# Optimization experiments

Measured on AMD Instinct MI355X. Metric: run time of the kernel, lower is better.

## Reference

```python
import jax, jax.numpy as jnp
import numpy as np

H = 16  # num_heads (d_model=1024, d_head=64)


def setup_inputs() -> dict:
    key = jax.random.key(0)
    ks = jax.random.split(key, 10)
    B, L, S, G, D = 8, 1024, 1024, 64, 1024
    s = 0.02  # keep score magnitudes sane for softmax
    return {
        "queries": jax.random.normal(ks[0], (B, L, D), jnp.float32),
        "keys": jax.random.normal(ks[1], (B, S, D), jnp.float32),
        "values": jax.random.normal(ks[2], (B, S, D), jnp.float32),
        "routers": jax.random.normal(ks[3], (B, G, D), jnp.float32),
        "Wq": jax.random.normal(ks[4], (D, D), jnp.float32) * s,
        "Wk": jax.random.normal(ks[5], (D, D), jnp.float32) * s,
        "Wv": jax.random.normal(ks[6], (D, D), jnp.float32) * s,
        "Wlq": jax.random.normal(ks[7], (D, D), jnp.float32) * s,
        "Wlk": jax.random.normal(ks[8], (D, D), jnp.float32) * s,
        "Wo": jax.random.normal(ks[9], (D, D), jnp.float32) * s,
        "bo": jnp.zeros((D,), jnp.float32),
    }


def reference(queries, keys, values, routers, Wq, Wk, Wv, Wlq, Wlk, Wo, bo):
    B, L, _ = queries.shape
    S = keys.shape[1]
    d_head = queries.shape[-1] // H
    scale = d_head ** (-0.5)

    def split_heads(x, W, n):
        # (B,n,d_model) @ (d_model,H*d_head) -> (B,H,n,d_head)
        return (x @ W).reshape(B, n, H, d_head).transpose(0, 2, 1, 3)

    q = split_heads(queries, Wq, L)
    k = split_heads(keys, Wk, S)
    v = split_heads(values, Wv, S)
    rq = split_heads(routers, Wlq, routers.shape[1])
    rk = split_heads(routers, Wlk, routers.shape[1])

    # learned per-head bilinear electrode-position matrix: (B,H,d,d)
    W_ep = jnp.einsum('bhgd,bhge->bhde', rq, rk)
    # bilinear QK scores: q . W_ep . k^T
    scores = jnp.einsum('bhld,bhde,bhke->bhlk', q, W_ep, k) * scale
    attn = jax.nn.softmax(scores, axis=-1)  # (B,H,L,S)
    out = jnp.einsum('bhlk,bhkd->bhld', attn, v)  # (B,H,L,d_head)
    # faithful to original: transpose(-2,-1) then view(B,L,-1)
    out = jnp.swapaxes(out, -2, -1).reshape(B, L, H * d_head)
    return out @ Wo + bo
```

## Files before the change

### kernel.cpp

```cpp
#include <hip/hip_runtime.h>

typedef __bf16 bf16;
typedef short s8v __attribute__((ext_vector_type(8)));
typedef float f4v __attribute__((ext_vector_type(4)));
typedef bf16 bf4v __attribute__((ext_vector_type(4)));
typedef bf16 bf8v __attribute__((ext_vector_type(8)));

#define NH 16
#define BB 8
#define QWSCALE 0.18033688011112043f

__device__ __forceinline__ void glds16(void* lds, const void* g) {
    __builtin_amdgcn_global_load_lds(
        (const __attribute__((address_space(1))) unsigned int*)g,
        (__attribute__((address_space(3))) unsigned int*)lds, 16, 0, 0);
}

__global__ __launch_bounds__(256) void rgemm_k(
    const float* __restrict__ A, const float* __restrict__ W1, const float* __restrict__ W2,
    float* __restrict__ C1, float* __restrict__ C2)
{
    __shared__ float As[16][68];
    __shared__ float Bs[16][68];
    const int tid = threadIdx.x;
    const int bm = blockIdx.x;
    int bn = blockIdx.y;
    const float* W = (bn < 16) ? W1 : W2;
    float* C = (bn < 16) ? C1 : C2;
    if (bn >= 16) bn -= 16;
    const int n0 = bn * 64;

    const int ar = tid >> 2, ac = (tid & 3) * 4;
    const int br = tid >> 4, bc = (tid & 15) * 4;
    const int tr = (tid >> 4) * 4, tc = (tid & 15) * 4;

    float acc[4][4];
#pragma unroll
    for (int i = 0; i < 4; i++)
#pragma unroll
        for (int j = 0; j < 4; j++) acc[i][j] = 0.f;

    for (int kt = 0; kt < 1024; kt += 16) {
        float4 av = *(const float4*)&A[(size_t)(bm * 64 + ar) * 1024 + kt + ac];
        float4 bv = *(const float4*)&W[(size_t)(kt + br) * 1024 + n0 + bc];
        __syncthreads();
        As[ac + 0][ar] = av.x; As[ac + 1][ar] = av.y;
        As[ac + 2][ar] = av.z; As[ac + 3][ar] = av.w;
        *(float4*)&Bs[br][bc] = bv;
        __syncthreads();
#pragma unroll
        for (int k = 0; k < 16; k++) {
            float4 x = *(const float4*)&As[k][tr];
            float4 y = *(const float4*)&Bs[k][tc];
            float xv[4] = {x.x, x.y, x.z, x.w};
            float yv[4] = {y.x, y.y, y.z, y.w};
#pragma unroll
            for (int i = 0; i < 4; i++)
#pragma unroll
                for (int j = 0; j < 4; j++) acc[i][j] += xv[i] * yv[j];
        }
    }

#pragma unroll
    for (int i = 0; i < 4; i++) {
        float4 v = make_float4(acc[i][0], acc[i][1], acc[i][2], acc[i][3]);
        *(float4*)&C[((size_t)(bm * NH + bn) * 64 + tr + i) * 64 + tc] = v;
    }
}

__global__ __launch_bounds__(256) void wep_k(
    const float* __restrict__ RQ, const float* __restrict__ RK, float* __restrict__ WEP)
{
    const int bh = blockIdx.x;
    __shared__ float rqs[4096];
    __shared__ float rks[4096];
    const int tid = threadIdx.x;
    const float4* rq4 = (const float4*)(RQ + (size_t)bh * 4096);
    const float4* rk4 = (const float4*)(RK + (size_t)bh * 4096);
#pragma unroll
    for (int j = 0; j < 4; j++) {
        ((float4*)rqs)[tid + 256 * j] = rq4[tid + 256 * j];
        ((float4*)rks)[tid + 256 * j] = rk4[tid + 256 * j];
    }
    __syncthreads();
    const int dd = tid >> 2, q = (tid & 3) * 16;
    float acc[16];
#pragma unroll
    for (int i = 0; i < 16; i++) acc[i] = 0.f;
    for (int g = 0; g < 64; g++) {
        float a = rqs[g * 64 + dd];
#pragma unroll
        for (int i = 0; i < 16; i++) acc[i] += a * rks[g * 64 + q + i];
    }
    float* out = WEP + (size_t)bh * 4096 + dd * 64 + q;
#pragma unroll
    for (int i4 = 0; i4 < 4; i4++)
        *(float4*)&out[i4 * 4] =
            make_float4(acc[i4 * 4], acc[i4 * 4 + 1], acc[i4 * 4 + 2], acc[i4 * 4 + 3]);
}

__global__ __launch_bounds__(256) void wqwep_k(
    const float* __restrict__ Wq, const float* __restrict__ WEP,
    bf16* __restrict__ Thi, bf16* __restrict__ Tlo)
{
    const int b = blockIdx.x >> 4, h = blockIdx.x & 15;
    __shared__ float weps[4096];
    __shared__ float wqs[128 * 68];
    const int tid = threadIdx.x;
    const float4* wsrc = (const float4*)(WEP + (size_t)blockIdx.x * 4096);
#pragma unroll
    for (int it = 0; it < 4; it++)
        ((float4*)weps)[it * 256 + tid] = wsrc[it * 256 + tid];
    const int Dloc = tid >> 1, e0 = (tid & 1) * 32;
    for (int Dt = 0; Dt < 8; Dt++) {
        __syncthreads();
#pragma unroll
        for (int it = 0; it < 8; it++) {
            int g = it * 256 + tid;
            int r = g >> 4, c = (g & 15) * 4;
            *(float4*)&wqs[r * 68 + c] =
                *(const float4*)&Wq[(size_t)(Dt * 128 + r) * 1024 + h * 64 + c];
        }
        __syncthreads();
        float acc[32];
#pragma unroll
        for (int e = 0; e < 32; e++) acc[e] = 0.f;
        for (int d = 0; d < 64; d++) {
            float a = wqs[Dloc * 68 + d];
            const float* wr = &weps[d * 64 + e0];
#pragma unroll
            for (int e = 0; e < 32; e++) acc[e] += a * wr[e];
        }
        int D = Dt * 128 + Dloc;
        size_t row0 = (size_t)b * 1024 + h * 64 + e0;
#pragma unroll
        for (int e = 0; e < 32; e++) {
            float v = acc[e] * QWSCALE;
            bf16 hv = (bf16)v;
            Thi[(row0 + e) * 1024 + D] = hv;
            Tlo[(row0 + e) * 1024 + D] = (bf16)(v - (float)hv);
        }
    }
}

__global__ void split_cast_k(const float* __restrict__ x, bf16* __restrict__ hi,
                             bf16* __restrict__ lo, int n4)
{
    int idx = blockIdx.x * blockDim.x + threadIdx.x;
    int stride = gridDim.x * blockDim.x;
    for (int i = idx; i < n4; i += stride) {
        float4 v = ((const float4*)x)[i];
        bf4v h;
        h[0] = (bf16)v.x; h[1] = (bf16)v.y; h[2] = (bf16)v.z; h[3] = (bf16)v.w;
        ((bf4v*)hi)[i] = h;
        if (lo) {
            bf4v l;
            l[0] = (bf16)(v.x - (float)h[0]);
            l[1] = (bf16)(v.y - (float)h[1]);
            l[2] = (bf16)(v.z - (float)h[2]);
            l[3] = (bf16)(v.w - (float)h[3]);
            ((bf4v*)lo)[i] = l;
        }
    }
}

__global__ __launch_bounds__(256) void transw_k(const float* __restrict__ W,
                                                bf16* __restrict__ WT, bf16* __restrict__ WTlo)
{
    __shared__ float T[64 * 68];
    const int k0 = blockIdx.x * 64, n0 = blockIdx.y * 64;
    const int tid = threadIdx.x;
#pragma unroll
    for (int it = 0; it < 4; it++) {
        int g = it * 256 + tid;
        int r = g >> 4, c = (g & 15) * 4;
        *(float4*)&T[r * 68 + c] = *(const float4*)&W[(size_t)(k0 + r) * 1024 + n0 + c];
    }
    __syncthreads();
#pragma unroll
    for (int it = 0; it < 4; it++) {
        int g = it * 256 + tid;
        int n = g >> 4, k4 = (g & 15) * 4;
        bf4v o, ol;
#pragma unroll
        for (int t = 0; t < 4; t++) {
            float v = T[(k4 + t) * 68 + n];
            o[t] = (bf16)v;
            ol[t] = (bf16)(v - (float)o[t]);
        }
        *(bf4v*)&WT[(size_t)(n0 + n) * 1024 + k0 + k4] = o;
        if (WTlo) *(bf4v*)&WTlo[(size_t)(n0 + n) * 1024 + k0 + k4] = ol;
    }
}

template<int PASSES>
__global__ __launch_bounds__(256, 2) void gemm_k(
    const bf16* __restrict__ A, const bf16* __restrict__ Alo,
    const bf16* __restrict__ Bt, const bf16* __restrict__ Btlo,
    int bBatched, int outmode,
    float* __restrict__ outF, const float* __restrict__ bias,
    bf16* __restrict__ outH, bf16* __restrict__ outL)
{
    __shared__ bf16 Ah[128 * 64];
    __shared__ bf16 Bh[128 * 64];
    __shared__ bf16 Al[(PASSES == 3) ? 128 * 64 : 64];
    __shared__ bf16 Bl[(PASSES == 3) ? 128 * 64 : 64];
    const int tid = threadIdx.x;
    const int bm = blockIdx.x, bn = blockIdx.y;
    const size_t boff = bBatched ? ((size_t)(bm >> 3) << 20) : (size_t)0;
    const bf16* Bt_b = Bt + boff;
    const bf16* Btlo_b = (PASSES == 3) ? (Btlo + boff) : nullptr;
    const int li = tid & 15;
    const int qq = (tid >> 4) & 3;
    const int wave = tid >> 6;
    const int wm0 = (wave & 1) * 64, wn0 = (wave >> 1) * 64;

    f4v acc[4][4];
    f4v zf; zf[0] = 0.f; zf[1] = 0.f; zf[2] = 0.f; zf[3] = 0.f;
#pragma unroll
    for (int mt = 0; mt < 4; mt++)
#pragma unroll
        for (int nt = 0; nt < 4; nt++) acc[mt][nt] = zf;

    for (int kt = 0; kt < 16; kt++) {
        const int col0 = kt * 64;
#pragma unroll
        for (int it = 0; it < 4; it++) {
            int g = it * 256 + tid;
            int r = g >> 3, p = g & 7;
            int gcol = col0 + ((p ^ (r & 7)) << 3);
            int ldsoff = (g & ~63) << 3;
            size_t ga = (size_t)(bm * 128 + r) * 1024 + gcol;
            size_t gb = (size_t)(bn * 128 + r) * 1024 + gcol;
            glds16(Ah + ldsoff, A + ga);
            glds16(Bh + ldsoff, Bt_b + gb);
            if (PASSES == 3) {
                glds16(Al + ldsoff, Alo + ga);
                glds16(Bl + ldsoff, Btlo_b + gb);
            }
        }
        __syncthreads();
#pragma unroll
        for (int ks = 0; ks < 2; ks++) {
            s8v af[4], alf[4], bhf[4], blf[4];
#pragma unroll
            for (int mt = 0; mt < 4; mt++) {
                int row = wm0 + mt * 16 + li;
                int off = row * 64 + (((ks * 4 + qq) ^ (li & 7)) << 3);
                af[mt] = *(const s8v*)&Ah[off];
                if (PASSES == 3) alf[mt] = *(const s8v*)&Al[off];
            }
#pragma unroll
            for (int nt = 0; nt < 4; nt++) {
                int row = wn0 + nt * 16 + li;
                int off = row * 64 + (((ks * 4 + qq) ^ (li & 7)) << 3);
                bhf[nt] = *(const s8v*)&Bh[off];
                if (PASSES == 3) blf[nt] = *(const s8v*)&Bl[off];
            }
#pragma unroll
            for (int mt = 0; mt < 4; mt++)
#pragma unroll
                for (int nt = 0; nt < 4; nt++) {
                    acc[mt][nt] = __builtin_amdgcn_mfma_f32_16x16x32_bf16(
                        af[mt], bhf[nt], acc[mt][nt], 0, 0, 0);
                    if (PASSES == 3) {
                        acc[mt][nt] = __builtin_amdgcn_mfma_f32_16x16x32_bf16(
                            alf[mt], bhf[nt], acc[mt][nt], 0, 0, 0);
                        acc[mt][nt] = __builtin_amdgcn_mfma_f32_16x16x32_bf16(
                            af[mt], blf[nt], acc[mt][nt], 0, 0, 0);
                    }
                }
        }
        __syncthreads();
    }

#pragma unroll
    for (int mt = 0; mt < 4; mt++) {
#pragma unroll
        for (int nt = 0; nt < 4; nt++) {
            int n = bn * 128 + wn0 + nt * 16 + li;
            int m0 = bm * 128 + wm0 + mt * 16 + qq * 4;
            if (outmode == 0) {
                float bv = bias[n];
#pragma unroll
                for (int rg = 0; rg < 4; rg++)
                    outF[(size_t)(m0 + rg) * 1024 + n] = acc[mt][nt][rg] + bv;
            } else if (outmode == 1) {
                int h = n >> 6, e = n & 63;
#pragma unroll
                for (int rg = 0; rg < 4; rg++) {
                    int m = m0 + rg;
                    int b = m >> 10, l = m & 1023;
                    size_t idx = ((size_t)(b * NH + h) * 1024 + l) * 64 + e;
                    float v = acc[mt][nt][rg];
                    bf16 hv = (bf16)v;
                    outH[idx] = hv;
                    outL[idx] = (bf16)(v - (float)hv);
                }
            } else {
                int b = m0 >> 10, s = m0 & 1023;
                int h = n >> 6, d = n & 63;
                bf4v v;
                v[0] = (bf16)acc[mt][nt][0]; v[1] = (bf16)acc[mt][nt][1];
                v[2] = (bf16)acc[mt][nt][2]; v[3] = (bf16)acc[mt][nt][3];
                *(bf4v*)&outH[((size_t)(b * NH + h) * 64 + d) * 1024 + s] = v;
            }
        }
    }
}

__global__ __launch_bounds__(256, 2) void attn_k(
    const bf16* __restrict__ QwHi, const bf16* __restrict__ QwLo,
    const bf16* __restrict__ KpHi, const bf16* __restrict__ KpLo,
    const bf16* __restrict__ VT, bf16* __restrict__ O)
{
    __shared__ bf16 Qh[128 * 64];
    __shared__ bf16 Ql[128 * 64];
    __shared__ __align__(16) char scratch[43008];
    bf16* Kh = (bf16*)scratch;
    bf16* Kl = Kh + 4096;
    bf16* Vt = Kh + 8192;
    bf16* Pb = Kh + 12288;
    float* Obuf = (float*)scratch;

    const int tid = threadIdx.x;
    const int l0 = blockIdx.x * 128;
    const int bh = blockIdx.z * NH + blockIdx.y;
    const int li = tid & 15;
    const int qq = (tid >> 4) & 3;
    const int wave = tid >> 6;
    const int r0w = wave * 32;

    const bf16* qhsrc = QwHi + ((size_t)bh * 1024 + l0) * 64;
    const bf16* qlsrc = QwLo + ((size_t)bh * 1024 + l0) * 64;
#pragma unroll
    for (int it = 0; it < 8; it++) {
        int g = it * 256 + tid;
        int buf = g >> 10;
        int L = g & 1023;
        int r = L >> 3, p = L & 7;
        int goff = r * 64 + ((p ^ (r & 7)) << 3);
        glds16((buf ? Ql : Qh) + ((L & ~63) << 3), (buf ? qlsrc : qhsrc) + goff);
    }

    float mrun[2], lsum[2];
    mrun[0] = -__builtin_inff(); mrun[1] = -__builtin_inff();
    lsum[0] = 0.f; lsum[1] = 0.f;
    f4v accO[4][2];
    {
        f4v zf; zf[0] = 0.f; zf[1] = 0.f; zf[2] = 0.f; zf[3] = 0.f;
#pragma unroll
        for (int dt = 0; dt < 4; dt++) { accO[dt][0] = zf; accO[dt][1] = zf; }
    }

    for (int s0 = 0; s0 < 1024; s0 += 64) {
        __syncthreads();
#pragma unroll
        for (int it = 0; it < 6; it++) {
            int g = it * 256 + tid;
            int buf = g >> 9;
            int L = g & 511;
            int r = L >> 3, p = L & 7;
            int blk = (p ^ (r & 7)) << 3;
            const bf16* src;
            bf16* dstb;
            if (buf == 0)      { src = KpHi + ((size_t)bh * 1024 + s0 + r) * 64 + blk; dstb = Kh; }
            else if (buf == 1) { src = KpLo + ((size_t)bh * 1024 + s0 + r) * 64 + blk; dstb = Kl; }
            else               { src = VT + ((size_t)bh * 64 + r) * 1024 + s0 + blk;   dstb = Vt; }
            glds16(dstb + ((L & ~63) << 3), src);
        }
        __syncthreads();

        f4v accS[4][2];
        {
            f4v zf; zf[0] = 0.f; zf[1] = 0.f; zf[2] = 0.f; zf[3] = 0.f;
#pragma unroll
            for (int ct = 0; ct < 4; ct++) { accS[ct][0] = zf; accS[ct][1] = zf; }
        }
#pragma unroll
        for (int ks = 0; ks < 2; ks++) {
            s8v khf[4], klf[4], qhf[2], qlf[2];
#pragma unroll
            for (int ct = 0; ct < 4; ct++) {
                int row = ct * 16 + li;
                int off = row * 64 + (((ks * 4 + qq) ^ (li & 7)) << 3);
                khf[ct] = *(const s8v*)&Kh[off];
                klf[ct] = *(const s8v*)&Kl[off];
            }
#pragma unroll
            for (int rt = 0; rt < 2; rt++) {
                int row = r0w + rt * 16 + li;
                int off = row * 64 + (((ks * 4 + qq) ^ (li & 7)) << 3);
                qhf[rt] = *(const s8v*)&Qh[off];
                qlf[rt] = *(const s8v*)&Ql[off];
            }
#pragma unroll
            for (int ct = 0; ct < 4; ct++)
#pragma unroll
                for (int rt = 0; rt < 2; rt++) {
                    accS[ct][rt] = __builtin_amdgcn_mfma_f32_16x16x32_bf16(
                        khf[ct], qhf[rt], accS[ct][rt], 0, 0, 0);
                    accS[ct][rt] = __builtin_amdgcn_mfma_f32_16x16x32_bf16(
                        khf[ct], qlf[rt], accS[ct][rt], 0, 0, 0);
                    accS[ct][rt] = __builtin_amdgcn_mfma_f32_16x16x32_bf16(
                        klf[ct], qhf[rt], accS[ct][rt], 0, 0, 0);
                }
        }

#pragma unroll
        for (int rt = 0; rt < 2; rt++) {
            float mx = -1e30f;
#pragma unroll
            for (int ct = 0; ct < 4; ct++)
#pragma unroll
                for (int rg = 0; rg < 4; rg++) mx = fmaxf(mx, accS[ct][rt][rg]);
            mx = fmaxf(mx, __shfl_xor(mx, 16));
            mx = fmaxf(mx, __shfl_xor(mx, 32));
            float mnew = fmaxf(mrun[rt], mx);
            float alpha = exp2f(mrun[rt] - mnew);
            float ls = 0.f;
            int prow = r0w + rt * 16 + li;
#pragma unroll
            for (int ct = 0; ct < 4; ct++) {
                bf4v pv;
#pragma unroll
                for (int rg = 0; rg < 4; rg++) {
                    float p_ = exp2f(accS[ct][rt][rg] - mnew);
                    ls += p_;
                    pv[rg] = (bf16)p_;
                }
                *(bf4v*)&Pb[prow * 72 + ct * 16 + qq * 4] = pv;
            }
            ls += __shfl_xor(ls, 16);
            ls += __shfl_xor(ls, 32);
            lsum[rt] = lsum[rt] * alpha + ls;
            mrun[rt] = mnew;
#pragma unroll
            for (int dt = 0; dt < 4; dt++)
#pragma unroll
                for (int rg = 0; rg < 4; rg++) accO[dt][rt][rg] *= alpha;
        }
        asm volatile("" ::: "memory");

#pragma unroll
        for (int ks = 0; ks < 2; ks++) {
            s8v vf[4], pf[2];
#pragma unroll
            for (int dt = 0; dt < 4; dt++) {
                int row = dt * 16 + li;
                int off = row * 64 + (((ks * 4 + qq) ^ (li & 7)) << 3);
                vf[dt] = *(const s8v*)&Vt[off];
            }
#pragma unroll
            for (int rt = 0; rt < 2; rt++) {
                int row = r0w + rt * 16 + li;
                pf[rt] = *(const s8v*)&Pb[row * 72 + ks * 32 + qq * 8];
            }
#pragma unroll
            for (int dt = 0; dt < 4; dt++)
#pragma unroll
                for (int rt = 0; rt < 2; rt++)
                    accO[dt][rt] = __builtin_amdgcn_mfma_f32_16x16x32_bf16(
                        vf[dt], pf[rt], accO[dt][rt], 0, 0, 0);
        }
    }

    __syncthreads();
#pragma unroll
    for (int rt = 0; rt < 2; rt++) {
        float inv = 1.f / lsum[rt];
        int rr = r0w + rt * 16 + li;
#pragma unroll
        for (int dt = 0; dt < 4; dt++)
#pragma unroll
            for (int rg = 0; rg < 4; rg++)
                Obuf[(dt * 16 + qq * 4 + rg) * 132 + rr] = accO[dt][rt][rg] * inv;
    }
    __syncthreads();
    {
        int d = tid >> 2, c0 = (tid & 3) * 32;
        const float* src = &Obuf[d * 132 + c0];
        bf16* dst = O + ((size_t)blockIdx.z * 1024 + blockIdx.y * 64 + d) * 1024 + l0 + c0;
#pragma unroll
        for (int q8 = 0; q8 < 4; q8++) {
            bf8v o;
#pragma unroll
            for (int j = 0; j < 8; j++) o[j] = (bf16)src[q8 * 8 + j];
            *(bf8v*)&dst[q8 * 8] = o;
        }
    }
}

extern "C" void kernel_launch(void* const* d_in, const int* in_sizes, int n_in,
                              void* d_out, int out_size, void* d_ws, size_t ws_size,
                              hipStream_t stream) {
    const float* queries = (const float*)d_in[0];
    const float* keys    = (const float*)d_in[1];
    const float* values  = (const float*)d_in[2];
    const float* routers = (const float*)d_in[3];
    const float* Wq  = (const float*)d_in[4];
    const float* Wk  = (const float*)d_in[5];
    const float* Wv  = (const float*)d_in[6];
    const float* Wlq = (const float*)d_in[7];
    const float* Wlk = (const float*)d_in[8];
    const float* Wo  = (const float*)d_in[9];
    const float* bo  = (const float*)d_in[10];
    float* out = (float*)d_out;

    char* w = (char*)d_ws;
    const size_t BIG = 16777216;
    bf16* QwHi = (bf16*)(w);
    bf16* QwLo = (bf16*)(w + 1 * BIG);
    bf16* Thi  = (bf16*)(w + 2 * BIG);
    bf16* Tlo  = (bf16*)(w + 3 * BIG);
    bf16* actHi = (bf16*)(w + 4 * BIG);
    bf16* actLo = (bf16*)(w + 5 * BIG);
    char* w2 = w + 6 * BIG;
    const size_t SM = 2097152;
    bf16*  WkThi = (bf16*)(w2);
    bf16*  WkTlo = (bf16*)(w2 + 1 * SM);
    bf16*  WvT   = (bf16*)(w2 + 2 * SM);
    bf16*  WoT   = (bf16*)(w2 + 3 * SM);
    float* RQ    = (float*)(w2 + 4 * SM);
    float* RK    = (float*)(w2 + 5 * SM);
    float* WEP   = (float*)(w2 + 6 * SM);
    bf16* KpHi = Thi;
    bf16* KpLo = Tlo;
    bf16* VTp  = actLo;
    bf16* Obf  = actHi;

    dim3 blk(256);
    transw_k<<<dim3(16, 16), blk, 0, stream>>>(Wk, WkThi, WkTlo);
    transw_k<<<dim3(16, 16), blk, 0, stream>>>(Wv, WvT, nullptr);
    transw_k<<<dim3(16, 16), blk, 0, stream>>>(Wo, WoT, nullptr);
    rgemm_k<<<dim3(8, 32), blk, 0, stream>>>(routers, Wlq, Wlk, RQ, RK);
    wep_k<<<dim3(BB * NH), blk, 0, stream>>>(RQ, RK, WEP);
    wqwep_k<<<dim3(BB * NH), blk, 0, stream>>>(Wq, WEP, Thi, Tlo);
    split_cast_k<<<1024, blk, 0, stream>>>(queries, actHi, actLo, 2097152);
    gemm_k<3><<<dim3(64, 8), blk, 0, stream>>>(actHi, actLo, Thi, Tlo, 1, 1,
                                               nullptr, nullptr, QwHi, QwLo);
    split_cast_k<<<1024, blk, 0, stream>>>(keys, actHi, actLo, 2097152);
    gemm_k<3><<<dim3(64, 8), blk, 0, stream>>>(actHi, actLo, WkThi, WkTlo, 0, 1,
                                               nullptr, nullptr, KpHi, KpLo);
    split_cast_k<<<1024, blk, 0, stream>>>(values, actHi, nullptr, 2097152);
    gemm_k<1><<<dim3(64, 8), blk, 0, stream>>>(actHi, nullptr, WvT, nullptr, 0, 2,
                                               nullptr, nullptr, VTp, nullptr);
    attn_k<<<dim3(8, NH, BB), blk, 0, stream>>>(QwHi, QwLo, KpHi, KpLo, VTp, Obf);
    gemm_k<1><<<dim3(64, 8), blk, 0, stream>>>(Obf, nullptr, WoT, nullptr, 0, 0,
                                               out, bo, nullptr, nullptr);
}
```

Baseline: 638.9 us.

## Split wqwep kernel over D tiles and coalesce bf16 hi/lo stores via LDS

The Wq·W_ep fold kernel now launches one block per (batch-head, D-tile) instead of looping over eight D tiles inside a single block, which multiplies the grid from 128 to 1024 blocks. Results are first staged in shared memory as packed hi/lo bf16 pairs and then written with 16-byte vector stores along contiguous D. The old path did scattered 2-byte strided stores. Each block now reloads the W_ep tile, which adds redundant reads, plus one extra LDS round trip.

```diff
diff --git a/kernel.cpp b/kernel.cpp
--- a/kernel.cpp
+++ b/kernel.cpp
@@ -103,42 +103,63 @@
     const float* __restrict__ Wq, const float* __restrict__ WEP,
     bf16* __restrict__ Thi, bf16* __restrict__ Tlo)
 {
-    const int b = blockIdx.x >> 4, h = blockIdx.x & 15;
+    const int bh = blockIdx.x;
+    const int b = bh >> 4, h = bh & 15;
+    const int Dt = blockIdx.y;
     __shared__ float weps[4096];
     __shared__ float wqs[128 * 68];
     const int tid = threadIdx.x;
-    const float4* wsrc = (const float4*)(WEP + (size_t)blockIdx.x * 4096);
+    const float4* wsrc = (const float4*)(WEP + (size_t)bh * 4096);
 #pragma unroll
     for (int it = 0; it < 4; it++)
         ((float4*)weps)[it * 256 + tid] = wsrc[it * 256 + tid];
+#pragma unroll
+    for (int it = 0; it < 8; it++) {
+        int g = it * 256 + tid;
+        int r = g >> 4, c = (g & 15) * 4;
+        *(float4*)&wqs[r * 68 + c] =
+            *(const float4*)&Wq[(size_t)(Dt * 128 + r) * 1024 + h * 64 + c];
+    }
+    __syncthreads();
     const int Dloc = tid >> 1, e0 = (tid & 1) * 32;
-    for (int Dt = 0; Dt < 8; Dt++) {
-        __syncthreads();
-#pragma unroll
-        for (int it = 0; it < 8; it++) {
-            int g = it * 256 + tid;
-            int r = g >> 4, c = (g & 15) * 4;
-            *(float4*)&wqs[r * 68 + c] =
-                *(const float4*)&Wq[(size_t)(Dt * 128 + r) * 1024 + h * 64 + c];
-        }
-        __syncthreads();
-        float acc[32];
-#pragma unroll
-        for (int e = 0; e < 32; e++) acc[e] = 0.f;
-        for (int d = 0; d < 64; d++) {
-            float a = wqs[Dloc * 68 + d];
-            const float* wr = &weps[d * 64 + e0];
-#pragma unroll
-            for (int e = 0; e < 32; e++) acc[e] += a * wr[e];
-        }
-        int D = Dt * 128 + Dloc;
-        size_t row0 = (size_t)b * 1024 + h * 64 + e0;
-#pragma unroll
-        for (int e = 0; e < 32; e++) {
-            float v = acc[e] * QWSCALE;
-            bf16 hv = (bf16)v;
-            Thi[(row0 + e) * 1024 + D] = hv;
-            Tlo[(row0 + e) * 1024 + D] = (bf16)(v - (float)hv);
+    float acc[32];
+#pragma unroll
+    for (int e = 0; e < 32; e++) acc[e] = 0.f;
+    for (int d = 0; d < 64; d++) {
+        float a = wqs[Dloc * 68 + d];
+        const float* wr = &weps[d * 64 + e0];
+#pragma unroll
+        for (int e = 0; e < 32; e++) acc[e] += a * wr[e];
+    }
+    __syncthreads();
+    unsigned* stage = (unsigned*)wqs;
+#pragma unroll
+    for (int e = 0; e < 32; e++) {
+        float v = acc[e] * QWSCALE;
+        bf16 hv = (bf16)v;
+        bf16 lv = (bf16)(v - (float)hv);
+        unsigned hb = *(unsigned short*)&hv;
+        unsigned lb = *(unsigned short*)&lv;
+        stage[(e0 + e) * 132 + Dloc] = hb | (lb << 16);
+    }
+    __syncthreads();
+    {
+        const int e = tid >> 2, c0 = (tid & 3) * 32;
+        const unsigned* src = &stage[e * 132 + c0];
+        bf16 hi32[32], lo32[32];
+#pragma unroll
+        for (int j = 0; j < 32; j++) {
+            unsigned u = src[j];
+            unsigned short hb = (unsigned short)(u & 0xffff);
+            unsigned short lb = (unsigned short)(u >> 16);
+            hi32[j] = *(bf16*)&hb;
+            lo32[j] = *(bf16*)&lb;
+        }
+        size_t base = ((size_t)b * 1024 + h * 64 + e) * 1024 + Dt * 128 + c0;
+#pragma unroll
+        for (int q8 = 0; q8 < 4; q8++) {
+            *(bf8v*)&Thi[base + q8 * 8] = *(bf8v*)&hi32[q8 * 8];
+            *(bf8v*)&Tlo[base + q8 * 8] = *(bf8v*)&lo32[q8 * 8];
         }
     }
 }
@@ -535,7 +556,7 @@
     transw_k<<<dim3(16, 16), blk, 0, stream>>>(Wo, WoT, nullptr);
     rgemm_k<<<dim3(8, 32), blk, 0, stream>>>(routers, Wlq, Wlk, RQ, RK);
     wep_k<<<dim3(BB * NH), blk, 0, stream>>>(RQ, RK, WEP);
-    wqwep_k<<<dim3(BB * NH), blk, 0, stream>>>(Wq, WEP, Thi, Tlo);
+    wqwep_k<<<dim3(BB * NH, 8), blk, 0, stream>>>(Wq, WEP, Thi, Tlo);
     split_cast_k<<<1024, blk, 0, stream>>>(queries, actHi, actLo, 2097152);
     gemm_k<3><<<dim3(64, 8), blk, 0, stream>>>(actHi, actLo, Thi, Tlo, 1, 1,
                                                nullptr, nullptr, QwHi, QwLo);
```

Measured after the change: 553.3 us. 1.15x faster.
